# Kernel tuning notes

Hardware: AMD Instinct MI355X
Metric: run time of the kernel (lower is better)

## Reference

```python
import jax, jax.numpy as jnp
import numpy as np

K = 1024
H = 16

def setup_inputs() -> dict:
    key = jax.random.key(0)
    ks = jax.random.split(key, 6)
    s = 1.0 / np.sqrt(K)
    return {
        "x": jax.random.normal(ks[0], (2, 2048, K), dtype=jnp.float32),
        "Wq": jax.random.uniform(ks[1], (K, K), jnp.float32, -s, s),
        "Wk": jax.random.uniform(ks[2], (K, K), jnp.float32, -s, s),
        "Wv": jax.random.uniform(ks[3], (K, K), jnp.float32, -s, s),
        "Wu": jax.random.uniform(ks[4], (K, K), jnp.float32, -s, s),
        "bu": jax.random.uniform(ks[5], (K,), jnp.float32, -s, s),
    }

def reference(x, Wq, Wk, Wv, Wu, bu):
    b, t, k = x.shape
    hd = k // H  # head dim = 64
    scale = jnp.asarray(k, x.dtype) ** 0.25  # Bloem-style: scale q and k each by k^(1/4)
    # nn.Linear(bias=False): y = x @ W.T
    q = (jnp.einsum('btk,ok->bto', x, Wq) / scale).reshape(b, t, H, hd)
    kk = (jnp.einsum('btk,ok->bto', x, Wk) / scale).reshape(b, t, H, hd)
    v = jnp.einsum('btk,ok->bto', x, Wv).reshape(b, t, H, hd)
    dot = jnp.einsum('bthd,bshd->bhts', q, kk)  # [b,h,t,t]
    att = jax.nn.softmax(dot, axis=-1)
    out = jnp.einsum('bhts,bshd->bthd', att, v).reshape(b, t, k)
    return jnp.einsum('btk,ok->bto', out, Wu) + bu
```

## Files before the change

### kernel.cpp

```cpp
#include <hip/hip_runtime.h>

typedef __bf16 bf16;
typedef bf16  bf16x8 __attribute__((ext_vector_type(8)));
typedef bf16  bf16x4 __attribute__((ext_vector_type(4)));
typedef float f32x4  __attribute__((ext_vector_type(4)));
typedef unsigned int u32x2 __attribute__((ext_vector_type(2)));
typedef unsigned int u32x4 __attribute__((ext_vector_type(4)));

#define MFMA16(a, b, c) __builtin_amdgcn_mfma_f32_16x16x32_bf16((a), (b), (c), 0, 0, 0)
#define AS1 __attribute__((address_space(1)))
#define AS3 __attribute__((address_space(3)))

__device__ __forceinline__ void gld_lds16(const bf16* g, bf16* l) {
    __builtin_amdgcn_global_load_lds((AS1 void*)(g), (AS3 void*)(l), 16, 0, 0);
}


__global__ __launch_bounds__(256) void cvt_all(const float* __restrict__ x,
                                               const float* __restrict__ Wq, const float* __restrict__ Wk,
                                               const float* __restrict__ Wv, const float* __restrict__ Wu,
                                               bf16* ox, bf16* oq, bf16* ok, bf16* ov, bf16* ou,
                                               float sq, float sk) {
    int bid = blockIdx.x;
    const float* src; bf16* dst; float sc; int base;
    if (bid < 4096) { src = x; dst = ox; sc = 1.0f; base = bid; }
    else {
        int w = (bid - 4096) >> 10; base = (bid - 4096) & 1023;
        switch (w) {
            case 0:  src = Wq; dst = oq; sc = sq;   break;
            case 1:  src = Wk; dst = ok; sc = sk;   break;
            case 2:  src = Wv; dst = ov; sc = 1.0f; break;
            default: src = Wu; dst = ou; sc = 1.0f; break;
        }
    }
    int idx = (base * 256 + threadIdx.x) * 4;
    float4 v = *(const float4*)(src + idx);
    bf16x4 o;
    o[0] = (bf16)(v.x * sc); o[1] = (bf16)(v.y * sc);
    o[2] = (bf16)(v.z * sc); o[3] = (bf16)(v.w * sc);
    *(bf16x4*)(dst + idx) = o;
}

__device__ __forceinline__ void gemm_core(const bf16* __restrict__ A, const bf16* __restrict__ B,
                                          int mBase, int nBase, bf16* As, bf16* Bs,
                                          f32x4 acc[4][4]) {
    const int tid = threadIdx.x;
    const int wave = tid >> 6, lane = tid & 63;
    const int g = lane >> 4, lr = lane & 15;
    const int wm = (wave & 1) << 6, wn = (wave >> 1) << 6;
    const int q = lane >> 2;
    const int cswz = ((lane & 3) ^ ((lane >> 3) & 3)) << 3;
    const int pcs  = (g ^ ((lr >> 1) & 3)) << 3;

    const int rb0 = wave << 4, rb1 = rb0 + 64;
    const bf16* a0 = A + (size_t)(mBase + rb0 + q) * 1024 + cswz;
    const bf16* a1 = A + (size_t)(mBase + rb1 + q) * 1024 + cswz;
    const bf16* b0 = B + (size_t)(nBase + rb0 + q) * 1024 + cswz;
    const bf16* b1 = B + (size_t)(nBase + rb1 + q) * 1024 + cswz;

    for (int k0 = 0; k0 < 1024; k0 += 32) {
        __syncthreads();
        gld_lds16(a0 + k0, As + rb0 * 32);
        gld_lds16(a1 + k0, As + rb1 * 32);
        gld_lds16(b0 + k0, Bs + rb0 * 32);
        gld_lds16(b1 + k0, Bs + rb1 * 32);
        __syncthreads();

        bf16x8 af[4], bfr[4];
#pragma unroll
        for (int i = 0; i < 4; i++)
            af[i] = *(const bf16x8*)&As[(wm + (i << 4) + lr) * 32 + pcs];
#pragma unroll
        for (int j = 0; j < 4; j++)
            bfr[j] = *(const bf16x8*)&Bs[(wn + (j << 4) + lr) * 32 + pcs];
#pragma unroll
        for (int i = 0; i < 4; i++)
#pragma unroll
            for (int j = 0; j < 4; j++)
                acc[i][j] = MFMA16(af[i], bfr[j], acc[i][j]);
    }
}

__global__ __launch_bounds__(256) void gemm_qkv(const bf16* __restrict__ X,
                                                const bf16* __restrict__ Wqk,
                                                const bf16* __restrict__ Wv,
                                                bf16* __restrict__ Qo, bf16* __restrict__ Ko,
                                                bf16* __restrict__ Vto) {
    __shared__ bf16 As[128 * 32];
    __shared__ bf16 Bs[128 * 32];
    const int tid = threadIdx.x;
    const int wave = tid >> 6, lane = tid & 63;
    const int g = lane >> 4, lr = lane & 15;
    const int wm = (wave & 1) << 6, wn = (wave >> 1) << 6;
    const int my = blockIdx.y;
    const bool qk = (my < 16);

    const bf16* Ap = qk ? Wqk : X;
    const bf16* Bp = qk ? X   : Wv;
    const int mBase = qk ? my * 128 : blockIdx.x * 128;
    const int nBase = qk ? blockIdx.x * 128 : (my - 16) * 128;

    f32x4 acc[4][4] = {};
    gemm_core(Ap, Bp, mBase, nBase, As, Bs, acc);

    if (qk) {
#pragma unroll
        for (int i = 0; i < 4; i++) {
            int m0 = mBase + wm + (i << 4) + (g << 2);
            bf16* dst = (m0 >> 10) ? Ko : Qo;
            int feat = m0 & 1023;
            int h = feat >> 6, d = feat & 63;
#pragma unroll
            for (int j = 0; j < 4; j++) {
                int t = nBase + wn + (j << 4) + lr;
                int b = t >> 11, tl = t & 2047;
                bf16x4 v;
#pragma unroll
                for (int r = 0; r < 4; r++) v[r] = (bf16)acc[i][j][r];
                *(bf16x4*)&dst[(((size_t)((b << 4) + h) * 2048 + tl) << 6) + d] = v;
            }
        }
    } else {
#pragma unroll
        for (int i = 0; i < 4; i++) {
            int t0 = mBase + wm + (i << 4) + (g << 2);
            int b = t0 >> 11, tl = t0 & 2047;
#pragma unroll
            for (int j = 0; j < 4; j++) {
                int o = nBase + wn + (j << 4) + lr;
                int h = o >> 6, d = o & 63;
                bf16x4 v;
#pragma unroll
                for (int r = 0; r < 4; r++) v[r] = (bf16)acc[i][j][r];
                *(bf16x4*)&Vto[((size_t)(((b << 4) + h) << 6) + d) * 2048 + tl] = v;
            }
        }
    }
}

__global__ __launch_bounds__(256) void gemm_out(const bf16* __restrict__ Wu, const bf16* __restrict__ A,
                                                const float* __restrict__ bias, float* __restrict__ out) {
    __shared__ bf16 As[128 * 32];
    __shared__ bf16 Bs[128 * 32];
    const int tid = threadIdx.x;
    const int wave = tid >> 6, lane = tid & 63;
    const int g = lane >> 4, lr = lane & 15;
    const int wm = (wave & 1) << 6, wn = (wave >> 1) << 6;
    const int mBase = blockIdx.y * 128, nBase = blockIdx.x * 128;

    f32x4 acc[4][4] = {};
    gemm_core(Wu, A, mBase, nBase, As, Bs, acc);

#pragma unroll
    for (int i = 0; i < 4; i++) {
        int o = mBase + wm + (i << 4) + (g << 2);
        float4 bv = *(const float4*)&bias[o];
#pragma unroll
        for (int j = 0; j < 4; j++) {
            int t = nBase + wn + (j << 4) + lr;
            float4 v;
            v.x = acc[i][j][0] + bv.x;
            v.y = acc[i][j][1] + bv.y;
            v.z = acc[i][j][2] + bv.z;
            v.w = acc[i][j][3] + bv.w;
            *(float4*)&out[((size_t)t << 10) + o] = v;
        }
    }
}

__global__ __launch_bounds__(256, 4) void attn(const bf16* __restrict__ Q, const bf16* __restrict__ Kt,
                                               const bf16* __restrict__ Vt, bf16* __restrict__ O) {
    __shared__ bf16 Qs[2][64][32];
    __shared__ bf16 Ks[2][128][32];
    __shared__ bf16 Vs[4][64][32];

    const int tid = threadIdx.x;
    const int wave = tid >> 6, lane = tid & 63;
    const int g = lane >> 4, lr = lane & 15;
    const int q = lane >> 2;
    const int cswz = ((lane & 3) ^ ((lane >> 3) & 3)) << 3;
    const int pcs  = (g ^ ((lr >> 1) & 3)) << 3;
    const int pair = wave >> 1;
    const int shalf = wave & 1;

    const int bid = blockIdx.x;
    const int bh = ((bid & 7) << 2) | (bid >> 8);
    const int qBase = ((bid >> 3) & 31) << 6;

    const bf16* Qg = Q + ((size_t)bh * 2048 + qBase) * 64;
    const bf16* Kg = Kt + (size_t)bh * 2048 * 64;
    const bf16* Vg = Vt + (size_t)bh * 64 * 2048;

#pragma unroll
    for (int i = 0; i < 2; i++) {
        int bi = (wave << 1) + i;
        int p = bi >> 2, rb = (bi & 3) << 4;
        gld_lds16(Qg + (rb + q) * 64 + (p << 5) + cswz, &Qs[p][rb][0]);
    }
    __syncthreads();

    bf16x8 qf[2][2];
#pragma unroll
    for (int ks = 0; ks < 2; ks++)
#pragma unroll
        for (int tt = 0; tt < 2; tt++)
            qf[ks][tt] = *(const bf16x8*)&Qs[ks][(pair << 5) + (tt << 4) + lr][pcs];

    bf16x8 ones;
#pragma unroll
    for (int i = 0; i < 8; i++) ones[i] = (bf16)1.0f;

    f32x4 oacc[2][4] = {};
    f32x4 oaccL[2] = {};

    for (int s0 = 0; s0 < 2048; s0 += 128) {
        __syncthreads();
#pragma unroll
        for (int i = 0; i < 4; i++) {
            int bi = (wave << 2) + i;
            {
                int p = bi >> 3, rb = (bi & 7) << 4;
                gld_lds16(Kg + (size_t)(s0 + rb + q) * 64 + (p << 5) + cswz, &Ks[p][rb][0]);
            }
            {
                int p = bi >> 2, rb = (bi & 3) << 4;
                gld_lds16(Vg + (size_t)(rb + q) * 2048 + s0 + (p << 5) + cswz, &Vs[p][rb][0]);
            }
        }
        __syncthreads();

#pragma unroll
        for (int sblk = 0; sblk < 2; sblk++) {
            f32x4 sacc[2][2] = {};
#pragma unroll
            for (int ks = 0; ks < 2; ks++)
#pragma unroll
                for (int isub = 0; isub < 2; isub++) {
                    bf16x8 kf = *(const bf16x8*)
                        &Ks[ks][(shalf << 6) + (sblk << 5) + (isub << 4) + lr][pcs];
                    sacc[isub][0] = MFMA16(kf, qf[ks][0], sacc[isub][0]);
                    sacc[isub][1] = MFMA16(kf, qf[ks][1], sacc[isub][1]);
                }
            bf16x8 pf[2];
#pragma unroll
            for (int tt = 0; tt < 2; tt++) {
                bf16x4 e0, e1;
#pragma unroll
                for (int r = 0; r < 4; r++) {
                    e0[r] = (bf16)__builtin_amdgcn_exp2f(sacc[0][tt][r]);
                    e1[r] = (bf16)__builtin_amdgcn_exp2f(sacc[1][tt][r]);
                }
                u32x2 a = __builtin_bit_cast(u32x2, e0);
                u32x2 b = __builtin_bit_cast(u32x2, e1);
                u32x2 t0  = __builtin_amdgcn_permlane32_swap(a.x, b.x, false, false);
                u32x2 w02 = __builtin_amdgcn_permlane16_swap(t0.x, t0.y, false, false);
                u32x2 t1  = __builtin_amdgcn_permlane32_swap(a.y, b.y, false, false);
                u32x2 w13 = __builtin_amdgcn_permlane16_swap(t1.x, t1.y, false, false);
                u32x4 w = {w02.x, w13.x, w02.y, w13.y};
                pf[tt] = __builtin_bit_cast(bf16x8, w);
            }
#pragma unroll
            for (int jd = 0; jd < 4; jd++) {
                bf16x8 vf = *(const bf16x8*)&Vs[(shalf << 1) + sblk][(jd << 4) + lr][pcs];
                oacc[0][jd] = MFMA16(pf[0], vf, oacc[0][jd]);
                oacc[1][jd] = MFMA16(pf[1], vf, oacc[1][jd]);
            }
            oaccL[0] = MFMA16(pf[0], ones, oaccL[0]);
            oaccL[1] = MFMA16(pf[1], ones, oaccL[1]);
        }
    }

    __syncthreads();
    float* Odump = (float*)&Ks[0][0][0];
    float* Ldump = (float*)&Vs[0][0][0];
    if (shalf == 1) {
#pragma unroll
        for (int tt = 0; tt < 2; tt++) {
#pragma unroll
            for (int jd = 0; jd < 4; jd++)
                *(f32x4*)&Odump[(pair << 11) + (((tt << 2) + jd) << 8) + (lane << 2)] = oacc[tt][jd];
            *(f32x4*)&Ldump[(pair << 9) + (tt << 8) + (lane << 2)] = oaccL[tt];
        }
    }
    __syncthreads();
    if (shalf == 0) {
        const int b = bh >> 4, h = bh & 15;
#pragma unroll
        for (int tt = 0; tt < 2; tt++) {
            f32x4 Lp = *(const f32x4*)&Ldump[(pair << 9) + (tt << 8) + (lane << 2)];
            f32x4 Ls = oaccL[tt] + Lp;
            float linv[4];
#pragma unroll
            for (int r = 0; r < 4; r++) linv[r] = 1.0f / Ls[r];
#pragma unroll
            for (int jd = 0; jd < 4; jd++) {
                f32x4 Op = *(const f32x4*)&Odump[(pair << 11) + (((tt << 2) + jd) << 8) + (lane << 2)];
                f32x4 v = oacc[tt][jd] + Op;
#pragma unroll
                for (int r = 0; r < 4; r++) {
                    int t = qBase + (pair << 5) + (tt << 4) + (g << 2) + r;
                    int col = (h << 6) + (jd << 4) + lr;
                    O[(((size_t)(b * 2048 + t)) << 10) + col] = (bf16)(v[r] * linv[r]);
                }
            }
        }
    }
}

extern "C" void kernel_launch(void* const* d_in, const int* in_sizes, int n_in,
                              void* d_out, int out_size, void* d_ws, size_t ws_size,
                              hipStream_t stream) {
    const float* x  = (const float*)d_in[0];
    const float* Wq = (const float*)d_in[1];
    const float* Wk = (const float*)d_in[2];
    const float* Wv = (const float*)d_in[3];
    const float* Wu = (const float*)d_in[4];
    const float* bu = (const float*)d_in[5];
    float* out = (float*)d_out;

    char* ws = (char*)d_ws;
    bf16* xbf  = (bf16*)(ws);
    bf16* wqbf = (bf16*)(ws + ((size_t)8  << 20));
    bf16* wkbf = (bf16*)(ws + ((size_t)10 << 20));
    bf16* wvbf = (bf16*)(ws + ((size_t)12 << 20));
    bf16* wubf = (bf16*)(ws + ((size_t)14 << 20));
    bf16* Qb   = (bf16*)(ws + ((size_t)16 << 20));
    bf16* Kb   = (bf16*)(ws + ((size_t)24 << 20));
    bf16* Vtb  = (bf16*)(ws + ((size_t)32 << 20));
    bf16* attnO = xbf;

    const float iscale_k = 0.17677669529663687f;
    const float iscale_q = 0.25503540109f;

    cvt_all<<<8192, 256, 0, stream>>>(x, Wq, Wk, Wv, Wu, xbf, wqbf, wkbf, wvbf, wubf,
                                      iscale_q, iscale_k);

    gemm_qkv<<<dim3(32, 24), 256, 0, stream>>>(xbf, wqbf, wvbf, Qb, Kb, Vtb);
    attn<<<dim3(1024), 256, 0, stream>>>(Qb, Kb, Vtb, attnO);
    gemm_out<<<dim3(32, 8), 256, 0, stream>>>(wubf, attnO, bu, out);
}
```

Measured before the change: 181.7 us.

## Split attention key range across four waves, each covering all 64 queries

Each wave now handles all 64 query rows against its own 32-key slice of every 128-key tile. Before, the waves were paired and each covered 32 queries against 64 keys. This halves the per-wave LDS reads of K and V fragments relative to MFMA work and removes the inner sblk loop. In exchange the accumulator registers double, so the occupancy hint drops from 4 to 2 blocks. The final cross-wave reduction becomes a three-phase LDS tree with extra barriers.

```diff
diff --git a/kernel.cpp b/kernel.cpp
--- a/kernel.cpp
+++ b/kernel.cpp
@@ -168,7 +168,7 @@
     }
 }
 
-__global__ __launch_bounds__(256, 4) void attn(const bf16* __restrict__ Q, const bf16* __restrict__ Kt,
+__global__ __launch_bounds__(256, 2) void attn(const bf16* __restrict__ Q, const bf16* __restrict__ Kt,
                                                const bf16* __restrict__ Vt, bf16* __restrict__ O) {
     __shared__ bf16 Qs[2][64][32];
     __shared__ bf16 Ks[2][128][32];
@@ -180,8 +180,6 @@
     const int q = lane >> 2;
     const int cswz = ((lane & 3) ^ ((lane >> 3) & 3)) << 3;
     const int pcs  = (g ^ ((lr >> 1) & 3)) << 3;
-    const int pair = wave >> 1;
-    const int shalf = wave & 1;
 
     const int bid = blockIdx.x;
     const int bh = ((bid & 7) << 2) | (bid >> 8);
@@ -199,19 +197,19 @@
     }
     __syncthreads();
 
-    bf16x8 qf[2][2];
+    bf16x8 qf[2][4];
 #pragma unroll
     for (int ks = 0; ks < 2; ks++)
 #pragma unroll
-        for (int tt = 0; tt < 2; tt++)
-            qf[ks][tt] = *(const bf16x8*)&Qs[ks][(pair << 5) + (tt << 4) + lr][pcs];
+        for (int tt = 0; tt < 4; tt++)
+            qf[ks][tt] = *(const bf16x8*)&Qs[ks][(tt << 4) + lr][pcs];
 
     bf16x8 ones;
 #pragma unroll
     for (int i = 0; i < 8; i++) ones[i] = (bf16)1.0f;
 
-    f32x4 oacc[2][4] = {};
-    f32x4 oaccL[2] = {};
+    f32x4 oacc[4][4] = {};
+    f32x4 oaccL[4] = {};
 
     for (int s0 = 0; s0 < 2048; s0 += 128) {
         __syncthreads();
@@ -229,76 +227,110 @@
         }
         __syncthreads();
 
-#pragma unroll
-        for (int sblk = 0; sblk < 2; sblk++) {
-            f32x4 sacc[2][2] = {};
-#pragma unroll
-            for (int ks = 0; ks < 2; ks++)
-#pragma unroll
-                for (int isub = 0; isub < 2; isub++) {
-                    bf16x8 kf = *(const bf16x8*)
-                        &Ks[ks][(shalf << 6) + (sblk << 5) + (isub << 4) + lr][pcs];
-                    sacc[isub][0] = MFMA16(kf, qf[ks][0], sacc[isub][0]);
-                    sacc[isub][1] = MFMA16(kf, qf[ks][1], sacc[isub][1]);
-                }
-            bf16x8 pf[2];
-#pragma unroll
-            for (int tt = 0; tt < 2; tt++) {
-                bf16x4 e0, e1;
+        f32x4 sacc[2][4] = {};
+#pragma unroll
+        for (int ks = 0; ks < 2; ks++)
+#pragma unroll
+            for (int isub = 0; isub < 2; isub++) {
+                bf16x8 kf = *(const bf16x8*)
+                    &Ks[ks][(wave << 5) + (isub << 4) + lr][pcs];
+#pragma unroll
+                for (int tt = 0; tt < 4; tt++)
+                    sacc[isub][tt] = MFMA16(kf, qf[ks][tt], sacc[isub][tt]);
+            }
+        bf16x8 pf[4];
+#pragma unroll
+        for (int tt = 0; tt < 4; tt++) {
+            bf16x4 e0, e1;
+#pragma unroll
+            for (int r = 0; r < 4; r++) {
+                e0[r] = (bf16)__builtin_amdgcn_exp2f(sacc[0][tt][r]);
+                e1[r] = (bf16)__builtin_amdgcn_exp2f(sacc[1][tt][r]);
+            }
+            u32x2 a = __builtin_bit_cast(u32x2, e0);
+            u32x2 b = __builtin_bit_cast(u32x2, e1);
+            u32x2 t0  = __builtin_amdgcn_permlane32_swap(a.x, b.x, false, false);
+            u32x2 w02 = __builtin_amdgcn_permlane16_swap(t0.x, t0.y, false, false);
+            u32x2 t1  = __builtin_amdgcn_permlane32_swap(a.y, b.y, false, false);
+            u32x2 w13 = __builtin_amdgcn_permlane16_swap(t1.x, t1.y, false, false);
+            u32x4 w = {w02.x, w13.x, w02.y, w13.y};
+            pf[tt] = __builtin_bit_cast(bf16x8, w);
+        }
+#pragma unroll
+        for (int jd = 0; jd < 4; jd++) {
+            bf16x8 vf = *(const bf16x8*)&Vs[wave][(jd << 4) + lr][pcs];
+#pragma unroll
+            for (int tt = 0; tt < 4; tt++)
+                oacc[tt][jd] = MFMA16(pf[tt], vf, oacc[tt][jd]);
+        }
+#pragma unroll
+        for (int tt = 0; tt < 4; tt++)
+            oaccL[tt] = MFMA16(pf[tt], ones, oaccL[tt]);
+    }
+
+    __syncthreads();
+    float* OA = (float*)&Ks[0][0][0];
+    float* OB = (float*)&Vs[0][0][0];
+    float* LA = (float*)&Qs[0][0][0];
+    float* LB = LA + 1024;
+
+    if (wave >= 2) {
+        float* Od = (wave == 2) ? OA : OB;
+        float* Ld = (wave == 2) ? LA : LB;
+#pragma unroll
+        for (int tt = 0; tt < 4; tt++) {
+#pragma unroll
+            for (int jd = 0; jd < 4; jd++)
+                *(f32x4*)&Od[(((tt << 2) + jd) << 8) + (lane << 2)] = oacc[tt][jd];
+            *(f32x4*)&Ld[(tt << 8) + (lane << 2)] = oaccL[tt];
+        }
+    }
+    __syncthreads();
+    if (wave < 2) {
+        const float* Os = (wave == 0) ? OA : OB;
+        const float* Ls = (wave == 0) ? LA : LB;
+#pragma unroll
+        for (int tt = 0; tt < 4; tt++) {
+#pragma unroll
+            for (int jd = 0; jd < 4; jd++)
+                oacc[tt][jd] += *(const f32x4*)&Os[(((tt << 2) + jd) << 8) + (lane << 2)];
+            oaccL[tt] += *(const f32x4*)&Ls[(tt << 8) + (lane << 2)];
+        }
+    }
+    __syncthreads();
+    if (wave < 2) {
+        float* Od = (wave == 1) ? OA : OB;
+        float* Ld = (wave == 1) ? LA : LB;
+        const int tb = (wave == 1) ? 0 : 2;
+#pragma unroll
+        for (int ti = 0; ti < 2; ti++) {
+#pragma unroll
+            for (int jd = 0; jd < 4; jd++)
+                *(f32x4*)&Od[(((ti << 2) + jd) << 8) + (lane << 2)] = oacc[tb + ti][jd];
+            *(f32x4*)&Ld[(ti << 8) + (lane << 2)] = oaccL[tb + ti];
+        }
+    }
+    __syncthreads();
+    if (wave < 2) {
+        const float* Os = (wave == 0) ? OA : OB;
+        const float* Ls = (wave == 0) ? LA : LB;
+        const int tb = (wave == 0) ? 0 : 2;
+        const int b = bh >> 4, h = bh & 15;
+#pragma unroll
+        for (int ti = 0; ti < 2; ti++) {
+            const int tt = tb + ti;
+            f32x4 Lp = *(const f32x4*)&Ls[(ti << 8) + (lane << 2)];
+            f32x4 Lsum = oaccL[tt] + Lp;
+            float linv[4];
+#pragma unroll
+            for (int r = 0; r < 4; r++) linv[r] = 1.0f / Lsum[r];
+#pragma unroll
+            for (int jd = 0; jd < 4; jd++) {
+                f32x4 Op = *(const f32x4*)&Os[(((ti << 2) + jd) << 8) + (lane << 2)];
+                f32x4 v = oacc[tt][jd] + Op;
 #pragma unroll
                 for (int r = 0; r < 4; r++) {
-                    e0[r] = (bf16)__builtin_amdgcn_exp2f(sacc[0][tt][r]);
-                    e1[r] = (bf16)__builtin_amdgcn_exp2f(sacc[1][tt][r]);
-                }
-                u32x2 a = __builtin_bit_cast(u32x2, e0);
-                u32x2 b = __builtin_bit_cast(u32x2, e1);
-                u32x2 t0  = __builtin_amdgcn_permlane32_swap(a.x, b.x, false, false);
-                u32x2 w02 = __builtin_amdgcn_permlane16_swap(t0.x, t0.y, false, false);
-                u32x2 t1  = __builtin_amdgcn_permlane32_swap(a.y, b.y, false, false);
-                u32x2 w13 = __builtin_amdgcn_permlane16_swap(t1.x, t1.y, false, false);
-                u32x4 w = {w02.x, w13.x, w02.y, w13.y};
-                pf[tt] = __builtin_bit_cast(bf16x8, w);
-            }
-#pragma unroll
-            for (int jd = 0; jd < 4; jd++) {
-                bf16x8 vf = *(const bf16x8*)&Vs[(shalf << 1) + sblk][(jd << 4) + lr][pcs];
-                oacc[0][jd] = MFMA16(pf[0], vf, oacc[0][jd]);
-                oacc[1][jd] = MFMA16(pf[1], vf, oacc[1][jd]);
-            }
-            oaccL[0] = MFMA16(pf[0], ones, oaccL[0]);
-            oaccL[1] = MFMA16(pf[1], ones, oaccL[1]);
-        }
-    }
-
-    __syncthreads();
-    float* Odump = (float*)&Ks[0][0][0];
-    float* Ldump = (float*)&Vs[0][0][0];
-    if (shalf == 1) {
-#pragma unroll
-        for (int tt = 0; tt < 2; tt++) {
-#pragma unroll
-            for (int jd = 0; jd < 4; jd++)
-                *(f32x4*)&Odump[(pair << 11) + (((tt << 2) + jd) << 8) + (lane << 2)] = oacc[tt][jd];
-            *(f32x4*)&Ldump[(pair << 9) + (tt << 8) + (lane << 2)] = oaccL[tt];
-        }
-    }
-    __syncthreads();
-    if (shalf == 0) {
-        const int b = bh >> 4, h = bh & 15;
-#pragma unroll
-        for (int tt = 0; tt < 2; tt++) {
-            f32x4 Lp = *(const f32x4*)&Ldump[(pair << 9) + (tt << 8) + (lane << 2)];
-            f32x4 Ls = oaccL[tt] + Lp;
-            float linv[4];
-#pragma unroll
-            for (int r = 0; r < 4; r++) linv[r] = 1.0f / Ls[r];
-#pragma unroll
-            for (int jd = 0; jd < 4; jd++) {
-                f32x4 Op = *(const f32x4*)&Odump[(pair << 11) + (((tt << 2) + jd) << 8) + (lane << 2)];
-                f32x4 v = oacc[tt][jd] + Op;
-#pragma unroll
-                for (int r = 0; r < 4; r++) {
-                    int t = qBase + (pair << 5) + (tt << 4) + (g << 2) + r;
+                    int t = qBase + (tt << 4) + (g << 2) + r;
                     int col = (h << 6) + (jd << 4) + lr;
                     O[(((size_t)(b * 2048 + t)) << 10) + col] = (bf16)(v[r] * linv[r]);
                 }
```

New measurement: 471.5 us. 159% more time.
